# Performance work log

Hardware: AMD Instinct MI355X
Metric: run time of the kernel (lower is better)

## Reference

```python
import jax, jax.numpy as jnp
import numpy as np

LATENT = 256
HIDDEN = 512
MAX_NODES = 64
TAU = 1.0
BATCH = 128
IDX_I, IDX_J = np.triu_indices(MAX_NODES, k=1)  # P = 2016 pairs
EPS = 1e-10


def fixed_positional_encoding(max_len, d_model):
    pos = np.arange(max_len)[:, None].astype(np.float32)
    div = np.exp(np.arange(0, d_model, 2).astype(np.float32) * (-np.log(10000.0) / d_model))
    pe = np.zeros((max_len, d_model), dtype=np.float32)
    pe[:, 0::2] = np.sin(pos * div)
    pe[:, 1::2] = np.cos(pos * div)
    return jnp.asarray(pe)


def setup_inputs() -> dict:
    key = jax.random.key(0)
    ks = jax.random.split(key, 20)

    def unif(k, shape, fan):
        bound = 1.0 / np.sqrt(fan)
        return jax.random.uniform(k, shape, jnp.float32, -bound, bound)

    inp = {}
    inp["z"] = jax.random.normal(ks[0], (BATCH, LATENT), jnp.float32)
    inp["n_nodes"] = jax.random.randint(ks[1], (BATCH,), 1, MAX_NODES + 1)  # lengths >= 1
    inp["n_edges"] = 100
    inp["gumbel_u"] = jax.random.uniform(ks[2], (BATCH, len(IDX_I), 2), jnp.float32)
    # learned params
    inp["emb"] = jax.random.normal(ks[3], (MAX_NODES, LATENT), jnp.float32)
    inp["pe"] = fixed_positional_encoding(MAX_NODES, LATENT)
    inp["W_pre"] = unif(ks[4], (LATENT, 2 * LATENT), 2 * LATENT)
    inp["b_pre"] = unif(ks[5], (LATENT,), 2 * LATENT)
    # GRU layer 0 (input LATENT) and layer 1 (input HIDDEN), torch layout [3H, in]/[3H, H]
    inp["Wih0"] = unif(ks[6], (3 * HIDDEN, LATENT), HIDDEN)
    inp["Whh0"] = unif(ks[7], (3 * HIDDEN, HIDDEN), HIDDEN)
    inp["bih0"] = unif(ks[8], (3 * HIDDEN,), HIDDEN)
    inp["bhh0"] = unif(ks[9], (3 * HIDDEN,), HIDDEN)
    inp["Wih1"] = unif(ks[10], (3 * HIDDEN, HIDDEN), HIDDEN)
    inp["Whh1"] = unif(ks[11], (3 * HIDDEN, HIDDEN), HIDDEN)
    inp["bih1"] = unif(ks[12], (3 * HIDDEN,), HIDDEN)
    inp["bhh1"] = unif(ks[13], (3 * HIDDEN,), HIDDEN)
    inp["node_W"] = unif(ks[14], (HIDDEN, HIDDEN), HIDDEN)
    inp["adj_W1"] = unif(ks[15], (HIDDEN, 2 * HIDDEN), 2 * HIDDEN)
    inp["adj_b1"] = unif(ks[16], (HIDDEN,), 2 * HIDDEN)
    inp["adj_W2"] = unif(ks[17], (2, HIDDEN), HIDDEN)
    inp["adj_b2"] = unif(ks[18], (2,), HIDDEN)
    return inp


def gru_layer(x, Wih, Whh, bih, bhh):
    # x: [B, T, D] -> outputs [B, T, H], torch GRU gate math
    xt = jnp.swapaxes(x, 0, 1)  # [T, B, D]
    gi_all = jnp.einsum("tbd,gd->tbg", xt, Wih) + bih  # precompute input gates
    H = Whh.shape[1]

    def step(h, gi):
        gh = h @ Whh.T + bhh
        ir, iz, inn = gi[:, :H], gi[:, H:2 * H], gi[:, 2 * H:]
        hr, hz, hn = gh[:, :H], gh[:, H:2 * H], gh[:, 2 * H:]
        r = jax.nn.sigmoid(ir + hr)
        zg = jax.nn.sigmoid(iz + hz)
        n = jnp.tanh(inn + r * hn)
        h_new = (1.0 - zg) * n + zg * h
        return h_new, h_new

    h0 = jnp.zeros((x.shape[0], H), x.dtype)
    _, ys = jax.lax.scan(step, h0, gi_all)
    return jnp.swapaxes(ys, 0, 1)  # [B, T, H]


def reference(z, n_nodes, n_edges, gumbel_u, emb, pe, W_pre, b_pre,
              Wih0, Whh0, bih0, bhh0, Wih1, Whh1, bih1, bhh1,
              node_W, adj_W1, adj_b1, adj_W2, adj_b2):
    B = z.shape[0]
    M = MAX_NODES
    # build RNN input: broadcast latent + sinusoidal PE, concat learned pos embedding
    seq = z[:, None, :] + pe[None]                              # [B, M, L]
    pos = jnp.broadcast_to(emb[None], (B, M, LATENT))           # [B, M, L]
    seq = jnp.concatenate([seq, pos], axis=-1)                  # [B, M, 2L]
    seq = seq @ W_pre.T + b_pre                                 # [B, M, L]
    mask = jnp.arange(M)[None, :] < n_nodes[:, None]            # [B, M]
    seq = seq * mask[:, :, None]
    # GRU (packed-sequence semantics == run full padded seq, zero padded outputs)
    h1 = gru_layer(seq, Wih0, Whh0, bih0, bhh0)
    rnn_out = gru_layer(h1, Wih1, Whh1, bih1, bhh1)
    rnn_out = rnn_out * mask[:, :, None]
    node_emb = rnn_out @ node_W.T                               # [B, M, H]
    # gather upper-triangle pairs -> MLP -> 2-way logits
    emb_i = node_emb[:, IDX_I, :]
    emb_j = node_emb[:, IDX_J, :]
    pair = jnp.concatenate([emb_i, emb_j], axis=-1)             # [B, P, 2H]
    hmid = jax.nn.relu(pair @ adj_W1.T + adj_b1)
    logits = hmid @ adj_W2.T + adj_b2                           # [B, P, 2]
    # gumbel-softmax, hard (straight-through)
    g = -jnp.log(-jnp.log(gumbel_u + EPS) + EPS)
    y_soft = jax.nn.softmax((logits + g) / TAU, axis=-1)
    y_hard = jax.nn.one_hot(jnp.argmax(y_soft, axis=-1), 2, dtype=y_soft.dtype)
    y = jax.lax.stop_gradient(y_hard - y_soft) + y_soft
    vals = y[..., 0]                                            # [B, P]
    # scatter into dense symmetric adjacency, mask by valid nodes
    adj = jnp.zeros((B, M, M), z.dtype).at[:, IDX_I, IDX_J].set(vals)
    adj = adj + jnp.swapaxes(adj, 1, 2)
    mask2d = (mask[:, :, None] & mask[:, None, :]).astype(adj.dtype)
    return adj * mask2d
```

## Files before the change

kernel.cpp:

```cpp
#include <hip/hip_runtime.h>
#include <math.h>

#define LATENT 256
#define HIDDEN 512
#define MAXN   64
#define BATCH  128
#define NPAIR  2016
#define G3     1536

#define HT_S   65536
#define WT_S   1048576

__global__ __launch_bounds__(256) void pre_kernel(
    const float* __restrict__ z, const float* __restrict__ pe,
    const float* __restrict__ emb, const float* __restrict__ W_pre,
    const float* __restrict__ b_pre, float* __restrict__ ZC,
    float* __restrict__ adj,
    const float* __restrict__ adj_W1, const float* __restrict__ node_W,
    float* __restrict__ WAB,
    const float* __restrict__ Whh0, const float* __restrict__ Wih1,
    const float* __restrict__ Whh1, float* __restrict__ WT)
{
  __shared__ float s1[256];
  __shared__ float s2[256];
  int blk = blockIdx.x;
  int o = threadIdx.x;
  if (blk < 192) {
    int row = blk;
    if (row < 32) {
      int x = row * 256 + o;
      int b = x >> 6, d = x & 63;
      adj[(size_t)b * 4096 + d * 65] = 0.f;
    }
    const float* wr = W_pre + (size_t)o * 512;
    if (row < 128) {
      s1[o] = z[row * 256 + o];
      __syncthreads();
      float acc = 0.f;
      #pragma unroll 8
      for (int k = 0; k < 256; k += 4) {
        float4 w4 = *(const float4*)(wr + k);
        float4 x4 = *(const float4*)(&s1[k]);
        acc += x4.x * w4.x; acc += x4.y * w4.y; acc += x4.z * w4.z; acc += x4.w * w4.w;
      }
      ZC[row * 256 + o] = acc;
    } else {
      int m = row - 128;
      s1[o] = pe[m * 256 + o];
      s2[o] = emb[m * 256 + o];
      __syncthreads();
      float acc = b_pre[o];
      #pragma unroll 8
      for (int k = 0; k < 256; k += 4) {
        float4 w4 = *(const float4*)(wr + k);
        float4 x4 = *(const float4*)(&s1[k]);
        acc += x4.x * w4.x; acc += x4.y * w4.y; acc += x4.z * w4.z; acc += x4.w * w4.w;
      }
      #pragma unroll 8
      for (int k = 0; k < 256; k += 4) {
        float4 w4 = *(const float4*)(wr + 256 + k);
        float4 x4 = *(const float4*)(&s2[k]);
        acc += x4.x * w4.x; acc += x4.y * w4.y; acc += x4.z * w4.z; acc += x4.w * w4.w;
      }
      ZC[row * 256 + o] = acc;
    }
  } else if (blk < 448) {
    int idx = blk - 192;
    int k = (idx & 1) * 256 + o;
    int o0 = ((idx >> 1) & 63) * 8;
    int sel = idx >> 7;
    const float* a1 = adj_W1 + (sel ? 512 : 0);
    float acc[8] = {0.f, 0.f, 0.f, 0.f, 0.f, 0.f, 0.f, 0.f};
    for (int j = 0; j < 512; j++) {
      float w = node_W[(size_t)j * 512 + k];
      #pragma unroll
      for (int oo = 0; oo < 8; oo++)
        acc[oo] += a1[(size_t)(o0 + oo) * 1024 + j] * w;
    }
    #pragma unroll
    for (int oo = 0; oo < 8; oo++)
      WAB[(size_t)(sel * 512 + o0 + oo) * 512 + k] = acc[oo];
  } else {
    int idx2 = blk - 448;
    int mat = idx2 / 96;
    int r0 = (idx2 % 96) * 16;
    const float* Wsrc = (mat == 0) ? Whh0 : (mat == 1) ? Wih1 : Whh1;
    int r = r0 + (o >> 4);
    int ofull = r & 511, g = r >> 9;
    int i = ofull >> 3, oo = ofull & 7;
    int k0 = (o & 15) * 32;
    const float* src = Wsrc + (size_t)r * 512 + k0;
    float* dst = WT + (size_t)mat * WT_S + (size_t)i * 16384 + oo * 4 + g;
    for (int k = 0; k < 32; k++)
      dst[(size_t)(k0 + k) * 32] = src[k];
  }
}

template<bool MASK>
__global__ __launch_bounds__(256) void gemm_kernel(
    const float* __restrict__ A, int lda,
    const float* __restrict__ W, int ldw,
    const float* __restrict__ bias,
    float* __restrict__ C, int ldc,
    int M, int N, int K,
    const int* __restrict__ n_nodes)
{
  __shared__ float As[16][136];
  __shared__ float Ws[16][136];
  const int tid = threadIdx.x;
  const int tx = tid & 15, ty = tid >> 4;
  const int row0 = blockIdx.x * 128, col0 = blockIdx.y * 128;

  float acc[8][8];
  #pragma unroll
  for (int i = 0; i < 8; i++)
    #pragma unroll
    for (int j = 0; j < 8; j++) acc[i][j] = 0.f;

  float4 va[2], vw[2];
  auto load_tile = [&](int k0) {
    #pragma unroll
    for (int s = 0; s < 2; s++) {
      int q = tid + 256 * s;
      int r = q >> 2;
      int c4 = (q & 3) << 2;
      int gm = row0 + r;
      float4 v = make_float4(0.f, 0.f, 0.f, 0.f);
      if (gm < M) {
        v = *(const float4*)(A + (size_t)gm * lda + k0 + c4);
        if (MASK) {
          int bb = gm >> 6, tt = gm & 63;
          if (tt >= n_nodes[bb]) v = make_float4(0.f, 0.f, 0.f, 0.f);
        }
      }
      va[s] = v;
      int gn = col0 + r;
      vw[s] = *(const float4*)(W + (size_t)gn * ldw + k0 + c4);
    }
  };

  load_tile(0);
  for (int k0 = 0; k0 < K; k0 += 16) {
    __syncthreads();
    #pragma unroll
    for (int s = 0; s < 2; s++) {
      int q = tid + 256 * s;
      int r = q >> 2, c4 = (q & 3) << 2;
      As[c4 + 0][r] = va[s].x; As[c4 + 1][r] = va[s].y; As[c4 + 2][r] = va[s].z; As[c4 + 3][r] = va[s].w;
      Ws[c4 + 0][r] = vw[s].x; Ws[c4 + 1][r] = vw[s].y; Ws[c4 + 2][r] = vw[s].z; Ws[c4 + 3][r] = vw[s].w;
    }
    __syncthreads();
    if (k0 + 16 < K) load_tile(k0 + 16);
    #pragma unroll
    for (int kk = 0; kk < 16; kk++) {
      float4 a0 = *(const float4*)&As[kk][ty * 8];
      float4 a1 = *(const float4*)&As[kk][ty * 8 + 4];
      float4 b0 = *(const float4*)&Ws[kk][tx * 8];
      float4 b1 = *(const float4*)&Ws[kk][tx * 8 + 4];
      float av[8] = {a0.x, a0.y, a0.z, a0.w, a1.x, a1.y, a1.z, a1.w};
      float bv[8] = {b0.x, b0.y, b0.z, b0.w, b1.x, b1.y, b1.z, b1.w};
      #pragma unroll
      for (int i = 0; i < 8; i++)
        #pragma unroll
        for (int j = 0; j < 8; j++)
          acc[i][j] += av[i] * bv[j];
    }
  }

  float bb[8];
  #pragma unroll
  for (int j = 0; j < 8; j++) bb[j] = bias ? bias[col0 + tx * 8 + j] : 0.f;
  #pragma unroll
  for (int i = 0; i < 8; i++) {
    int gm = row0 + ty * 8 + i;
    if (gm < M) {
      float* out = C + (size_t)gm * ldc + col0 + tx * 8;
      float4 o0 = make_float4(acc[i][0] + bb[0], acc[i][1] + bb[1], acc[i][2] + bb[2], acc[i][3] + bb[3]);
      float4 o1 = make_float4(acc[i][4] + bb[4], acc[i][5] + bb[5], acc[i][6] + bb[6], acc[i][7] + bb[7]);
      *(float4*)out = o0;
      *(float4*)(out + 4) = o1;
    }
  }
}

__global__ __launch_bounds__(512) void gru_v9_kernel(
    const float* __restrict__ WT,
    const float* __restrict__ ZCW,
    const float* __restrict__ bih0, const float* __restrict__ bhh0,
    const float* __restrict__ bih1, const float* __restrict__ bhh1,
    const int* __restrict__ n_nodes,
    float* __restrict__ Ht1, float* __restrict__ H2t,
    float* __restrict__ H2row, int s)
{
  __shared__ float p_s[8][3][8][32];
  const int tid = threadIdx.x;
  const int plane = blockIdx.y;
  const int osl = blockIdx.x & 63;
  const int o0 = osl << 3;
  const int b0 = (blockIdx.x >> 6) << 5;
  const int w = tid >> 6, l = tid & 63;
  const int bg = l & 7, rg = l >> 3;

  int t;
  if (plane == 0) { t = s;     if (t > 63) return; }
  else            { t = s - 1; if (t < 0)  return; }

  float acc[3][4] = {{0.f, 0.f, 0.f, 0.f}, {0.f, 0.f, 0.f, 0.f}, {0.f, 0.f, 0.f, 0.f}};

  if (plane == 0) {
    if (t > 0) {
      const float* hp_ = Ht1 + ((t - 1) & 3) * HT_S + b0 + bg * 4 + (size_t)(w << 6) * 128;
      const float* wp_ = WT + (size_t)osl * 16384 + (size_t)(w << 6) * 32 + rg * 4;
      #pragma unroll 8
      for (int k = 0; k < 64; k++) {
        float4 h4 = *(const float4*)(hp_ + (size_t)k * 128);
        float4 w4 = *(const float4*)(wp_ + (size_t)k * 32);
        acc[0][0] += h4.x * w4.x; acc[0][1] += h4.y * w4.x; acc[0][2] += h4.z * w4.x; acc[0][3] += h4.w * w4.x;
        acc[1][0] += h4.x * w4.y; acc[1][1] += h4.y * w4.y; acc[1][2] += h4.z * w4.y; acc[1][3] += h4.w * w4.y;
        acc[2][0] += h4.x * w4.z; acc[2][1] += h4.y * w4.z; acc[2][2] += h4.z * w4.z; acc[2][3] += h4.w * w4.z;
      }
    }
  } else {
    const bool isIn = (w < 4);
    const bool run = isIn || (t > 0);
    if (run) {
      const int kb = (w & 3) << 7;
      const float* wp_ = WT + (size_t)(isIn ? 1 : 2) * WT_S
                       + (size_t)osl * 16384 + (size_t)kb * 32 + rg * 4;
      const float* Hi = isIn ? (Ht1 + (t & 3) * HT_S)
                             : (H2t + ((t - 1) & 1) * HT_S);
      const float* hp_ = Hi + b0 + bg * 4 + (size_t)kb * 128;
      #pragma unroll 8
      for (int k = 0; k < 128; k++) {
        float4 h4 = *(const float4*)(hp_ + (size_t)k * 128);
        float4 w4 = *(const float4*)(wp_ + (size_t)k * 32);
        acc[0][0] += h4.x * w4.x; acc[0][1] += h4.y * w4.x; acc[0][2] += h4.z * w4.x; acc[0][3] += h4.w * w4.x;
        acc[1][0] += h4.x * w4.y; acc[1][1] += h4.y * w4.y; acc[1][2] += h4.z * w4.y; acc[1][3] += h4.w * w4.y;
        acc[2][0] += h4.x * w4.z; acc[2][1] += h4.y * w4.z; acc[2][2] += h4.z * w4.z; acc[2][3] += h4.w * w4.z;
      }
    }
  }

  *(float4*)&p_s[w][0][rg][bg * 4] = make_float4(acc[0][0], acc[0][1], acc[0][2], acc[0][3]);
  *(float4*)&p_s[w][1][rg][bg * 4] = make_float4(acc[1][0], acc[1][1], acc[1][2], acc[1][3]);
  *(float4*)&p_s[w][2][rg][bg * 4] = make_float4(acc[2][0], acc[2][1], acc[2][2], acc[2][3]);
  __syncthreads();

  if (tid < 256) {
    int b = tid & 31, oi = tid >> 5;
    const int B = b0 + b, O = o0 + oi;

    if (plane == 0) {
      float s0 = 0.f, s1 = 0.f, s2 = 0.f;
      #pragma unroll
      for (int ww = 0; ww < 8; ww++) {
        s0 += p_s[ww][0][oi][b];
        s1 += p_s[ww][1][oi][b];
        s2 += p_s[ww][2][oi][b];
      }
      bool mk = t < n_nodes[B];
      float zr = mk ? ZCW[(size_t)B * G3 + O]        + ZCW[(size_t)(128 + t) * G3 + O]        : 0.f;
      float zz = mk ? ZCW[(size_t)B * G3 + 512 + O]  + ZCW[(size_t)(128 + t) * G3 + 512 + O]  : 0.f;
      float zn = mk ? ZCW[(size_t)B * G3 + 1024 + O] + ZCW[(size_t)(128 + t) * G3 + 1024 + O] : 0.f;
      float ir = zr + bih0[O], iz = zz + bih0[512 + O], inn = zn + bih0[1024 + O];
      float hr = s0 + bhh0[O], hz = s1 + bhh0[512 + O], hn = s2 + bhh0[1024 + O];
      float rg_ = 1.f / (1.f + expf(-(ir + hr)));
      float zg  = 1.f / (1.f + expf(-(iz + hz)));
      float ng  = tanhf(inn + rg_ * hn);
      float hp = (t > 0) ? Ht1[((t - 1) & 3) * HT_S + O * 128 + B] : 0.f;
      Ht1[(t & 3) * HT_S + O * 128 + B] = (1.f - zg) * ng + zg * hp;
    } else {
      float gi0 = 0.f, gi1 = 0.f, gi2 = 0.f, gh0 = 0.f, gh1 = 0.f, gh2 = 0.f;
      #pragma unroll
      for (int ww = 0; ww < 4; ww++) {
        gi0 += p_s[ww][0][oi][b];
        gi1 += p_s[ww][1][oi][b];
        gi2 += p_s[ww][2][oi][b];
      }
      #pragma unroll
      for (int ww = 4; ww < 8; ww++) {
        gh0 += p_s[ww][0][oi][b];
        gh1 += p_s[ww][1][oi][b];
        gh2 += p_s[ww][2][oi][b];
      }
      float ir = gi0 + bih1[O], iz = gi1 + bih1[512 + O], inn = gi2 + bih1[1024 + O];
      float hr = gh0 + bhh1[O], hz = gh1 + bhh1[512 + O], hn = gh2 + bhh1[1024 + O];
      float rg_ = 1.f / (1.f + expf(-(ir + hr)));
      float zg  = 1.f / (1.f + expf(-(iz + hz)));
      float ng  = tanhf(inn + rg_ * hn);
      float hp = (t > 0) ? H2t[((t - 1) & 1) * HT_S + O * 128 + B] : 0.f;
      float hnew = (1.f - zg) * ng + zg * hp;
      H2t[(t & 1) * HT_S + O * 128 + B] = hnew;
      H2row[((size_t)(B * 64 + t)) * 512 + O] = hnew;
    }
  }
}

__global__ __launch_bounds__(256) void pair_kernel(
    const float* __restrict__ AB, const float* __restrict__ b1,
    const float* __restrict__ W2, const float* __restrict__ b2,
    const float* __restrict__ gu, const int* __restrict__ n_nodes,
    float* __restrict__ adj)
{
  int wid = blockIdx.x * 4 + (threadIdx.x >> 6);
  int lane = threadIdx.x & 63;
  int b = wid / NPAIR;
  int p = wid - b * NPAIR;

  float fp = (float)p;
  int i = (int)((127.0f - sqrtf(16129.0f - 8.0f * fp)) * 0.5f);
  if (i < 0) i = 0;
  if (i > 62) i = 62;
  while (i < 62 && (i + 1) * (126 - i) / 2 <= p) i++;
  while (i > 0 && i * (127 - i) / 2 > p) i--;
  int j = p - i * (127 - i) / 2 + i + 1;

  int n = n_nodes[b];
  if (i >= n || j >= n) {
    if (lane == 0) {
      adj[(size_t)b * 4096 + i * 64 + j] = 0.f;
      adj[(size_t)b * 4096 + j * 64 + i] = 0.f;
    }
    return;
  }

  const float* arow = AB + ((size_t)(b * 64 + i)) * 1024;
  const float* brow = AB + ((size_t)(b * 64 + j)) * 1024 + 512;
  int k0 = lane * 8;

  float4 a0 = *(const float4*)(arow + k0);
  float4 a1 = *(const float4*)(arow + k0 + 4);
  float4 q0 = *(const float4*)(brow + k0);
  float4 q1 = *(const float4*)(brow + k0 + 4);
  float4 c0 = *(const float4*)(b1 + k0);
  float4 c1 = *(const float4*)(b1 + k0 + 4);

  float h0 = fmaxf(a0.x + q0.x + c0.x, 0.f);
  float h1 = fmaxf(a0.y + q0.y + c0.y, 0.f);
  float h2 = fmaxf(a0.z + q0.z + c0.z, 0.f);
  float h3 = fmaxf(a0.w + q0.w + c0.w, 0.f);
  float h4 = fmaxf(a1.x + q1.x + c1.x, 0.f);
  float h5 = fmaxf(a1.y + q1.y + c1.y, 0.f);
  float h6 = fmaxf(a1.z + q1.z + c1.z, 0.f);
  float h7 = fmaxf(a1.w + q1.w + c1.w, 0.f);

  float4 w00 = *(const float4*)(W2 + k0);
  float4 w01 = *(const float4*)(W2 + k0 + 4);
  float4 w10 = *(const float4*)(W2 + 512 + k0);
  float4 w11 = *(const float4*)(W2 + 512 + k0 + 4);

  float acc0 = h0 * w00.x + h1 * w00.y + h2 * w00.z + h3 * w00.w
             + h4 * w01.x + h5 * w01.y + h6 * w01.z + h7 * w01.w;
  float acc1 = h0 * w10.x + h1 * w10.y + h2 * w10.z + h3 * w10.w
             + h4 * w11.x + h5 * w11.y + h6 * w11.z + h7 * w11.w;

  #pragma unroll
  for (int off = 32; off > 0; off >>= 1) {
    acc0 += __shfl_xor(acc0, off, 64);
    acc1 += __shfl_xor(acc1, off, 64);
  }

  if (lane == 0) {
    float s0 = acc0 + b2[0];
    float s1 = acc1 + b2[1];
    const float* u = gu + ((size_t)(b * NPAIR + p)) * 2;
    float g0 = -logf(-logf(u[0] + 1e-10f) + 1e-10f);
    float g1 = -logf(-logf(u[1] + 1e-10f) + 1e-10f);
    float val = ((s0 + g0) >= (s1 + g1)) ? 1.f : 0.f;
    adj[(size_t)b * 4096 + i * 64 + j] = val;
    adj[(size_t)b * 4096 + j * 64 + i] = val;
  }
}

extern "C" void kernel_launch(void* const* d_in, const int* in_sizes, int n_in,
                              void* d_out, int out_size, void* d_ws, size_t ws_size,
                              hipStream_t stream)
{
  (void)in_sizes; (void)n_in; (void)out_size; (void)ws_size;

  const float* z       = (const float*)d_in[0];
  const int*   n_nodes = (const int*)d_in[1];
  const float* gu      = (const float*)d_in[3];
  const float* emb     = (const float*)d_in[4];
  const float* pe      = (const float*)d_in[5];
  const float* W_pre   = (const float*)d_in[6];
  const float* b_pre   = (const float*)d_in[7];
  const float* Wih0    = (const float*)d_in[8];
  const float* Whh0    = (const float*)d_in[9];
  const float* bih0    = (const float*)d_in[10];
  const float* bhh0    = (const float*)d_in[11];
  const float* Wih1    = (const float*)d_in[12];
  const float* Whh1    = (const float*)d_in[13];
  const float* bih1    = (const float*)d_in[14];
  const float* bhh1    = (const float*)d_in[15];
  const float* node_W  = (const float*)d_in[16];
  const float* adj_W1  = (const float*)d_in[17];
  const float* adj_b1  = (const float*)d_in[18];
  const float* adj_W2  = (const float*)d_in[19];
  const float* adj_b2  = (const float*)d_in[20];
  float* adj = (float*)d_out;

  char* ws = (char*)d_ws;
  float* ZC    = (float*)(ws + 0);
  float* ZCW   = (float*)(ws + 196608);
  float* WAB   = (float*)(ws + 1376256);
  float* WT    = (float*)(ws + 3473408);
  float* Ht1   = (float*)(ws + 16056320);
  float* H2t   = (float*)(ws + 17104896);
  float* H2row = (float*)(ws + 17629184);
  float* AB    = (float*)(ws + 34406400);

  pre_kernel<<<736, 256, 0, stream>>>(z, pe, emb, W_pre, b_pre, ZC, adj,
                                      adj_W1, node_W, WAB,
                                      Whh0, Wih1, Whh1, WT);

  gemm_kernel<false><<<dim3(2, 12), 256, 0, stream>>>(
      ZC, 256, Wih0, 256, nullptr, ZCW, 1536, 192, 1536, 256, nullptr);

  for (int s = 0; s <= 64; s++)
    gru_v9_kernel<<<dim3(256, 2), 512, 0, stream>>>(
        WT, ZCW, bih0, bhh0, bih1, bhh1, n_nodes,
        Ht1, H2t, H2row, s);

  gemm_kernel<true><<<dim3(64, 8), 256, 0, stream>>>(
      H2row, 512, WAB, 512, nullptr, AB, 1024, 8192, 1024, 512, n_nodes);

  pair_kernel<<<64512, 256, 0, stream>>>(AB, adj_b1, adj_W2, adj_b2, gu, n_nodes, adj);
}
```

Baseline: 2.064 ms.

## Fuse GRU timestep launches into one persistent cooperative kernel with grid barriers

Replaces the 65 per-timestep GRU launches with a single cooperative persistent kernel that loops over steps. Each block runs layer 0 and then layer 1 in sequence, and the 64 blocks sharing a batch slice synchronize through an atomic counter barrier. This removes the launch overhead and kernel-boundary drain on every step. The cost is serializing the two layers inside each block, where they used to run as separate planes, plus spin-wait barrier latency. If the cooperative launch fails, the code falls back to per-step launches.

```diff
diff --git a/kernel.cpp b/kernel.cpp
--- a/kernel.cpp
+++ b/kernel.cpp
@@ -183,115 +183,141 @@
   }
 }
 
-__global__ __launch_bounds__(512) void gru_v9_kernel(
+__global__ void bar_init_kernel(int* __restrict__ bar)
+{
+  if (threadIdx.x < 128) bar[threadIdx.x] = 0;
+}
+
+__global__ __launch_bounds__(512) void gru_v11_kernel(
     const float* __restrict__ WT,
     const float* __restrict__ ZCW,
     const float* __restrict__ bih0, const float* __restrict__ bhh0,
     const float* __restrict__ bih1, const float* __restrict__ bhh1,
     const int* __restrict__ n_nodes,
     float* __restrict__ Ht1, float* __restrict__ H2t,
-    float* __restrict__ H2row, int s)
+    float* __restrict__ H2row, int* __restrict__ bar,
+    int s0, int s1)
 {
   __shared__ float p_s[8][3][8][32];
   const int tid = threadIdx.x;
-  const int plane = blockIdx.y;
   const int osl = blockIdx.x & 63;
   const int o0 = osl << 3;
-  const int b0 = (blockIdx.x >> 6) << 5;
+  const int bsp = blockIdx.x >> 6;
+  const int b0 = bsp << 5;
   const int w = tid >> 6, l = tid & 63;
   const int bg = l & 7, rg = l >> 3;
-
-  int t;
-  if (plane == 0) { t = s;     if (t > 63) return; }
-  else            { t = s - 1; if (t < 0)  return; }
-
-  float acc[3][4] = {{0.f, 0.f, 0.f, 0.f}, {0.f, 0.f, 0.f, 0.f}, {0.f, 0.f, 0.f, 0.f}};
-
-  if (plane == 0) {
-    if (t > 0) {
-      const float* hp_ = Ht1 + ((t - 1) & 3) * HT_S + b0 + bg * 4 + (size_t)(w << 6) * 128;
-      const float* wp_ = WT + (size_t)osl * 16384 + (size_t)(w << 6) * 32 + rg * 4;
-      #pragma unroll 8
-      for (int k = 0; k < 64; k++) {
-        float4 h4 = *(const float4*)(hp_ + (size_t)k * 128);
-        float4 w4 = *(const float4*)(wp_ + (size_t)k * 32);
-        acc[0][0] += h4.x * w4.x; acc[0][1] += h4.y * w4.x; acc[0][2] += h4.z * w4.x; acc[0][3] += h4.w * w4.x;
-        acc[1][0] += h4.x * w4.y; acc[1][1] += h4.y * w4.y; acc[1][2] += h4.z * w4.y; acc[1][3] += h4.w * w4.y;
-        acc[2][0] += h4.x * w4.z; acc[2][1] += h4.y * w4.z; acc[2][2] += h4.z * w4.z; acc[2][3] += h4.w * w4.z;
-      }
-    }
-  } else {
-    const bool isIn = (w < 4);
-    const bool run = isIn || (t > 0);
-    if (run) {
-      const int kb = (w & 3) << 7;
-      const float* wp_ = WT + (size_t)(isIn ? 1 : 2) * WT_S
-                       + (size_t)osl * 16384 + (size_t)kb * 32 + rg * 4;
-      const float* Hi = isIn ? (Ht1 + (t & 3) * HT_S)
-                             : (H2t + ((t - 1) & 1) * HT_S);
-      const float* hp_ = Hi + b0 + bg * 4 + (size_t)kb * 128;
-      #pragma unroll 8
-      for (int k = 0; k < 128; k++) {
-        float4 h4 = *(const float4*)(hp_ + (size_t)k * 128);
-        float4 w4 = *(const float4*)(wp_ + (size_t)k * 32);
-        acc[0][0] += h4.x * w4.x; acc[0][1] += h4.y * w4.x; acc[0][2] += h4.z * w4.x; acc[0][3] += h4.w * w4.x;
-        acc[1][0] += h4.x * w4.y; acc[1][1] += h4.y * w4.y; acc[1][2] += h4.z * w4.y; acc[1][3] += h4.w * w4.y;
-        acc[2][0] += h4.x * w4.z; acc[2][1] += h4.y * w4.z; acc[2][2] += h4.z * w4.z; acc[2][3] += h4.w * w4.z;
-      }
-    }
-  }
-
-  *(float4*)&p_s[w][0][rg][bg * 4] = make_float4(acc[0][0], acc[0][1], acc[0][2], acc[0][3]);
-  *(float4*)&p_s[w][1][rg][bg * 4] = make_float4(acc[1][0], acc[1][1], acc[1][2], acc[1][3]);
-  *(float4*)&p_s[w][2][rg][bg * 4] = make_float4(acc[2][0], acc[2][1], acc[2][2], acc[2][3]);
-  __syncthreads();
-
-  if (tid < 256) {
-    int b = tid & 31, oi = tid >> 5;
-    const int B = b0 + b, O = o0 + oi;
-
-    if (plane == 0) {
-      float s0 = 0.f, s1 = 0.f, s2 = 0.f;
-      #pragma unroll
-      for (int ww = 0; ww < 8; ww++) {
-        s0 += p_s[ww][0][oi][b];
-        s1 += p_s[ww][1][oi][b];
-        s2 += p_s[ww][2][oi][b];
-      }
-      bool mk = t < n_nodes[B];
-      float zr = mk ? ZCW[(size_t)B * G3 + O]        + ZCW[(size_t)(128 + t) * G3 + O]        : 0.f;
-      float zz = mk ? ZCW[(size_t)B * G3 + 512 + O]  + ZCW[(size_t)(128 + t) * G3 + 512 + O]  : 0.f;
-      float zn = mk ? ZCW[(size_t)B * G3 + 1024 + O] + ZCW[(size_t)(128 + t) * G3 + 1024 + O] : 0.f;
-      float ir = zr + bih0[O], iz = zz + bih0[512 + O], inn = zn + bih0[1024 + O];
-      float hr = s0 + bhh0[O], hz = s1 + bhh0[512 + O], hn = s2 + bhh0[1024 + O];
-      float rg_ = 1.f / (1.f + expf(-(ir + hr)));
-      float zg  = 1.f / (1.f + expf(-(iz + hz)));
-      float ng  = tanhf(inn + rg_ * hn);
-      float hp = (t > 0) ? Ht1[((t - 1) & 3) * HT_S + O * 128 + B] : 0.f;
-      Ht1[(t & 3) * HT_S + O * 128 + B] = (1.f - zg) * ng + zg * hp;
-    } else {
-      float gi0 = 0.f, gi1 = 0.f, gi2 = 0.f, gh0 = 0.f, gh1 = 0.f, gh2 = 0.f;
-      #pragma unroll
-      for (int ww = 0; ww < 4; ww++) {
-        gi0 += p_s[ww][0][oi][b];
-        gi1 += p_s[ww][1][oi][b];
-        gi2 += p_s[ww][2][oi][b];
-      }
-      #pragma unroll
-      for (int ww = 4; ww < 8; ww++) {
-        gh0 += p_s[ww][0][oi][b];
-        gh1 += p_s[ww][1][oi][b];
-        gh2 += p_s[ww][2][oi][b];
-      }
-      float ir = gi0 + bih1[O], iz = gi1 + bih1[512 + O], inn = gi2 + bih1[1024 + O];
-      float hr = gh0 + bhh1[O], hz = gh1 + bhh1[512 + O], hn = gh2 + bhh1[1024 + O];
-      float rg_ = 1.f / (1.f + expf(-(ir + hr)));
-      float zg  = 1.f / (1.f + expf(-(iz + hz)));
-      float ng  = tanhf(inn + rg_ * hn);
-      float hp = (t > 0) ? H2t[((t - 1) & 1) * HT_S + O * 128 + B] : 0.f;
-      float hnew = (1.f - zg) * ng + zg * hp;
-      H2t[(t & 1) * HT_S + O * 128 + B] = hnew;
-      H2row[((size_t)(B * 64 + t)) * 512 + O] = hnew;
+  int* cnt = bar + bsp * 32;
+
+  for (int s = s0; s < s1; ++s) {
+    const int t0 = s;
+    if (t0 <= 63) {
+      float acc[3][4] = {{0.f,0.f,0.f,0.f},{0.f,0.f,0.f,0.f},{0.f,0.f,0.f,0.f}};
+      if (t0 > 0) {
+        const float* hp_ = Ht1 + ((t0 - 1) & 3) * HT_S + b0 + bg * 4 + (size_t)(w << 6) * 128;
+        const float* wp_ = WT + (size_t)osl * 16384 + (size_t)(w << 6) * 32 + rg * 4;
+        #pragma unroll 8
+        for (int k = 0; k < 64; k++) {
+          float4 h4 = *(const float4*)(hp_ + (size_t)k * 128);
+          float4 w4 = *(const float4*)(wp_ + (size_t)k * 32);
+          acc[0][0] += h4.x * w4.x; acc[0][1] += h4.y * w4.x; acc[0][2] += h4.z * w4.x; acc[0][3] += h4.w * w4.x;
+          acc[1][0] += h4.x * w4.y; acc[1][1] += h4.y * w4.y; acc[1][2] += h4.z * w4.y; acc[1][3] += h4.w * w4.y;
+          acc[2][0] += h4.x * w4.z; acc[2][1] += h4.y * w4.z; acc[2][2] += h4.z * w4.z; acc[2][3] += h4.w * w4.z;
+        }
+      }
+      *(float4*)&p_s[w][0][rg][bg * 4] = make_float4(acc[0][0], acc[0][1], acc[0][2], acc[0][3]);
+      *(float4*)&p_s[w][1][rg][bg * 4] = make_float4(acc[1][0], acc[1][1], acc[1][2], acc[1][3]);
+      *(float4*)&p_s[w][2][rg][bg * 4] = make_float4(acc[2][0], acc[2][1], acc[2][2], acc[2][3]);
+      __syncthreads();
+      if (tid < 256) {
+        int b = tid & 31, oi = tid >> 5;
+        const int B = b0 + b, O = o0 + oi;
+        float r0 = 0.f, r1 = 0.f, r2 = 0.f;
+        #pragma unroll
+        for (int ww = 0; ww < 8; ww++) {
+          r0 += p_s[ww][0][oi][b];
+          r1 += p_s[ww][1][oi][b];
+          r2 += p_s[ww][2][oi][b];
+        }
+        bool mk = t0 < n_nodes[B];
+        float zr = mk ? ZCW[(size_t)B * G3 + O]        + ZCW[(size_t)(128 + t0) * G3 + O]        : 0.f;
+        float zz = mk ? ZCW[(size_t)B * G3 + 512 + O]  + ZCW[(size_t)(128 + t0) * G3 + 512 + O]  : 0.f;
+        float zn = mk ? ZCW[(size_t)B * G3 + 1024 + O] + ZCW[(size_t)(128 + t0) * G3 + 1024 + O] : 0.f;
+        float ir = zr + bih0[O], iz = zz + bih0[512 + O], inn = zn + bih0[1024 + O];
+        float hr = r0 + bhh0[O], hz = r1 + bhh0[512 + O], hn = r2 + bhh0[1024 + O];
+        float rg_ = 1.f / (1.f + expf(-(ir + hr)));
+        float zg  = 1.f / (1.f + expf(-(iz + hz)));
+        float ng  = tanhf(inn + rg_ * hn);
+        float hp = (t0 > 0) ? Ht1[((t0 - 1) & 3) * HT_S + O * 128 + B] : 0.f;
+        Ht1[(t0 & 3) * HT_S + O * 128 + B] = (1.f - zg) * ng + zg * hp;
+      }
+    }
+
+    __syncthreads();
+
+    const int t1 = s - 1;
+    if (t1 >= 0) {
+      float acc[3][4] = {{0.f,0.f,0.f,0.f},{0.f,0.f,0.f,0.f},{0.f,0.f,0.f,0.f}};
+      const bool isIn = (w < 4);
+      const bool run = isIn || (t1 > 0);
+      if (run) {
+        const int kb = (w & 3) << 7;
+        const float* wp_ = WT + (size_t)(isIn ? 1 : 2) * WT_S
+                         + (size_t)osl * 16384 + (size_t)kb * 32 + rg * 4;
+        const float* Hi = isIn ? (Ht1 + (t1 & 3) * HT_S)
+                               : (H2t + ((t1 - 1) & 1) * HT_S);
+        const float* hp_ = Hi + b0 + bg * 4 + (size_t)kb * 128;
+        #pragma unroll 8
+        for (int k = 0; k < 128; k++) {
+          float4 h4 = *(const float4*)(hp_ + (size_t)k * 128);
+          float4 w4 = *(const float4*)(wp_ + (size_t)k * 32);
+          acc[0][0] += h4.x * w4.x; acc[0][1] += h4.y * w4.x; acc[0][2] += h4.z * w4.x; acc[0][3] += h4.w * w4.x;
+          acc[1][0] += h4.x * w4.y; acc[1][1] += h4.y * w4.y; acc[1][2] += h4.z * w4.y; acc[1][3] += h4.w * w4.y;
+          acc[2][0] += h4.x * w4.z; acc[2][1] += h4.y * w4.z; acc[2][2] += h4.z * w4.z; acc[2][3] += h4.w * w4.z;
+        }
+      }
+      *(float4*)&p_s[w][0][rg][bg * 4] = make_float4(acc[0][0], acc[0][1], acc[0][2], acc[0][3]);
+      *(float4*)&p_s[w][1][rg][bg * 4] = make_float4(acc[1][0], acc[1][1], acc[1][2], acc[1][3]);
+      *(float4*)&p_s[w][2][rg][bg * 4] = make_float4(acc[2][0], acc[2][1], acc[2][2], acc[2][3]);
+      __syncthreads();
+      if (tid < 256) {
+        int b = tid & 31, oi = tid >> 5;
+        const int B = b0 + b, O = o0 + oi;
+        float gi0 = 0.f, gi1 = 0.f, gi2 = 0.f, gh0 = 0.f, gh1 = 0.f, gh2 = 0.f;
+        #pragma unroll
+        for (int ww = 0; ww < 4; ww++) {
+          gi0 += p_s[ww][0][oi][b];
+          gi1 += p_s[ww][1][oi][b];
+          gi2 += p_s[ww][2][oi][b];
+        }
+        #pragma unroll
+        for (int ww = 4; ww < 8; ww++) {
+          gh0 += p_s[ww][0][oi][b];
+          gh1 += p_s[ww][1][oi][b];
+          gh2 += p_s[ww][2][oi][b];
+        }
+        float ir = gi0 + bih1[O], iz = gi1 + bih1[512 + O], inn = gi2 + bih1[1024 + O];
+        float hr = gh0 + bhh1[O], hz = gh1 + bhh1[512 + O], hn = gh2 + bhh1[1024 + O];
+        float rg_ = 1.f / (1.f + expf(-(ir + hr)));
+        float zg  = 1.f / (1.f + expf(-(iz + hz)));
+        float ng  = tanhf(inn + rg_ * hn);
+        float hp = (t1 > 0) ? H2t[((t1 - 1) & 1) * HT_S + O * 128 + B] : 0.f;
+        float hnew = (1.f - zg) * ng + zg * hp;
+        H2t[(t1 & 1) * HT_S + O * 128 + B] = hnew;
+        H2row[((size_t)(B * 64 + t1)) * 512 + O] = hnew;
+      }
+    }
+
+    if (s < s1 - 1) {
+      __threadfence();
+      __syncthreads();
+      if (tid == 0) {
+        __hip_atomic_fetch_add(cnt, 1, __ATOMIC_RELEASE, __HIP_MEMORY_SCOPE_AGENT);
+        const int target = 64 * (s + 1);
+        while (__hip_atomic_load(cnt, __ATOMIC_ACQUIRE, __HIP_MEMORY_SCOPE_AGENT) < target)
+          __builtin_amdgcn_s_sleep(8);
+      }
+      __syncthreads();
+      __threadfence();
     }
   }
 }
@@ -409,6 +435,7 @@
   float* H2t   = (float*)(ws + 17104896);
   float* H2row = (float*)(ws + 17629184);
   float* AB    = (float*)(ws + 34406400);
+  int*   bar   = (int*)(ws + 67960832);
 
   pre_kernel<<<736, 256, 0, stream>>>(z, pe, emb, W_pre, b_pre, ZC, adj,
                                       adj_W1, node_W, WAB,
@@ -417,10 +444,26 @@
   gemm_kernel<false><<<dim3(2, 12), 256, 0, stream>>>(
       ZC, 256, Wih0, 256, nullptr, ZCW, 1536, 192, 1536, 256, nullptr);
 
-  for (int s = 0; s <= 64; s++)
-    gru_v9_kernel<<<dim3(256, 2), 512, 0, stream>>>(
-        WT, ZCW, bih0, bhh0, bih1, bhh1, n_nodes,
-        Ht1, H2t, H2row, s);
+  bar_init_kernel<<<1, 128, 0, stream>>>(bar);
+
+  {
+    int cs0 = 0, cs1 = 65;
+    void* a[13];
+    a[0] = (void*)&WT;   a[1] = (void*)&ZCW;  a[2] = (void*)&bih0;
+    a[3] = (void*)&bhh0; a[4] = (void*)&bih1; a[5] = (void*)&bhh1;
+    a[6] = (void*)&n_nodes; a[7] = (void*)&Ht1; a[8] = (void*)&H2t;
+    a[9] = (void*)&H2row; a[10] = (void*)&bar; a[11] = (void*)&cs0;
+    a[12] = (void*)&cs1;
+    hipError_t ce = hipLaunchCooperativeKernel((const void*)&gru_v11_kernel,
+                                               dim3(256, 1, 1), dim3(512, 1, 1),
+                                               a, 0, stream);
+    if (ce != hipSuccess) {
+      for (int s = 0; s <= 64; s++)
+        gru_v11_kernel<<<dim3(256, 1, 1), 512, 0, stream>>>(
+            WT, ZCW, bih0, bhh0, bih1, bhh1, n_nodes,
+            Ht1, H2t, H2row, bar, s, s + 1);
+    }
+  }
 
   gemm_kernel<true><<<dim3(64, 8), 256, 0, stream>>>(
       H2row, 512, WAB, 512, nullptr, AB, 1024, 8192, 1024, 512, n_nodes);
```

Result: slower. 7.028 ms (+240.5%).
